# Kernel tuning notes

Hardware: AMD Instinct MI355X
Metric: run time of the kernel (lower is better)

## Reference

```python
import jax, jax.numpy as jnp
import numpy as np

N_NODE = 100000
N_EDGE = 1600000
D_FEAT = 32
DEPTH = 10
BASE_ALPHA = 1.0


def setup_inputs() -> dict:
    key = jax.random.key(0)
    k1, k2, k3, k4 = jax.random.split(key, 4)
    x = jax.random.normal(k1, (N_NODE, D_FEAT), dtype=jnp.float32)
    edge_index = jax.random.randint(k2, (2, N_EDGE), 0, N_NODE, dtype=jnp.int64)
    edge_attr = jax.random.uniform(k3, (N_EDGE,), dtype=jnp.float32)
    pe_alphas = jax.random.normal(k4, (DEPTH,), dtype=jnp.float32)
    return {"x": x, "edge_index": edge_index, "edge_attr": edge_attr, "pe_alphas": pe_alphas}


def reference(x, edge_index, edge_attr, pe_alphas):
    n = x.shape[0]
    row, col = edge_index[0], edge_index[1]
    # GCN normalization: deg from row (source of each edge), clamp isolated nodes
    deg = jax.ops.segment_sum(jnp.ones_like(edge_attr), row, num_segments=n)
    deg = jnp.where(deg < 0.5, deg + 1.0, deg)
    dinv = deg ** -0.5
    val = dinv[row] * edge_attr * dinv[col]  # [E]

    alphas = BASE_ALPHA * jnp.tanh(pe_alphas)  # [DEPTH]

    def spmm(h):  # adj @ h via gather + segment-sum scatter
        return jax.ops.segment_sum(val[:, None] * h[col], row, num_segments=n)

    # PowerConv (monomial basis): x_L = alpha_{L-1} * (adj @ x_{L-1}), x_0 = x
    def step(h, a):
        nh = a * spmm(h)
        return nh, nh

    _, ys = jax.lax.scan(step, x, alphas)  # ys: [DEPTH, n, d]
    out = jnp.concatenate([x[None], ys], axis=0)  # [DEPTH+1, n, d]
    return jnp.moveaxis(out, 0, 1)  # [n, DEPTH+1, d]
```

## Files before the change

### kernel.cpp

```cpp
#include <hip/hip_runtime.h>

#define NN 100000
#define NE 1600000
#define DF 32
#define DEPTH 10
#define LSTRIDE ((DEPTH + 1) * DF)
#define SCAN_BLOCKS 256
#define SCAN_T 256
#define PAD 8
#define PADM (~(PAD - 1))

__global__ void zcnt_k(int* __restrict__ cnt, int n4) {
    int i = blockIdx.x * blockDim.x + threadIdx.x;
    if (i < n4) ((int4*)cnt)[i] = make_int4(0, 0, 0, 0);
}

__global__ void hist_k(const int* __restrict__ row, int* __restrict__ cnt,
                       int* __restrict__ prank, int e) {
    int i = blockIdx.x * blockDim.x + threadIdx.x;
    int stride = gridDim.x * blockDim.x;
    for (; i < e; i += stride) {
        int r = __builtin_nontemporal_load(&row[i]);
        prank[i] = atomicAdd(&cnt[r], 1);
    }
}

__global__ void scan_partial_k(const int* __restrict__ cnt, int* __restrict__ bsum,
                               int n, int chunk) {
    __shared__ int red[SCAN_T];
    int b = blockIdx.x, t = threadIdx.x;
    int beg = b * chunk, end = min(n, beg + chunk);
    int s = 0;
    for (int i = beg + t; i < end; i += SCAN_T) s += (cnt[i] + PAD - 1) & PADM;
    red[t] = s;
    __syncthreads();
    for (int off = SCAN_T / 2; off; off >>= 1) {
        if (t < off) red[t] += red[t + off];
        __syncthreads();
    }
    if (t == 0) bsum[b] = red[0];
}

__global__ void scan_bsum_k(const int* __restrict__ bsum, int* __restrict__ boff) {
    __shared__ int s[SCAN_BLOCKS];
    int t = threadIdx.x;
    s[t] = bsum[t];
    __syncthreads();
    for (int off = 1; off < SCAN_BLOCKS; off <<= 1) {
        int v = (t >= off) ? s[t - off] : 0;
        __syncthreads();
        s[t] += v;
        __syncthreads();
    }
    boff[t] = (t == 0) ? 0 : s[t - 1];
}

__global__ void scan_emit_k(const int* __restrict__ cnt, const int* __restrict__ boff,
                            int* __restrict__ rowptr, float* __restrict__ dinv,
                            int n, int chunk) {
    __shared__ int tile[SCAN_T];
    int b = blockIdx.x, t = threadIdx.x;
    int beg = b * chunk, end = min(n, beg + chunk);
    int run = boff[b];
    for (int base = beg; base < end; base += SCAN_T) {
        int i = base + t;
        int creal = (i < end) ? cnt[i] : 0;
        int c = (creal + PAD - 1) & PADM;
        tile[t] = c;
        __syncthreads();
        for (int off = 1; off < SCAN_T; off <<= 1) {
            int v = (t >= off) ? tile[t - off] : 0;
            __syncthreads();
            tile[t] += v;
            __syncthreads();
        }
        if (i < end) {
            rowptr[i] = run + tile[t] - c;
            float d = (creal == 0) ? 1.0f : (float)creal;
            dinv[i] = rsqrtf(d);
        }
        run += tile[SCAN_T - 1];
        __syncthreads();
    }
    if (b == gridDim.x - 1 && t == 0) rowptr[n] = run;
}

__global__ void pad_k(const int* __restrict__ rowptr, const int* __restrict__ cnt,
                      unsigned long long* __restrict__ cpack, int n) {
    int r = blockIdx.x * blockDim.x + threadIdx.x;
    if (r < n) {
        int p = rowptr[r] + cnt[r];
        int end = rowptr[r + 1];
        for (; p < end; ++p) cpack[p] = 0ull;
    }
}

__global__ void scatter_k(const int* __restrict__ row, const int* __restrict__ col,
                          const float* __restrict__ ea, const float* __restrict__ dinv,
                          const int* __restrict__ rowptr, const int* __restrict__ prank,
                          unsigned long long* __restrict__ cpack, int e) {
    int i = blockIdx.x * blockDim.x + threadIdx.x;
    int stride = gridDim.x * blockDim.x;
    for (; i < e; i += stride) {
        int r = __builtin_nontemporal_load(&row[i]);
        int c = __builtin_nontemporal_load(&col[i]);
        float a = __builtin_nontemporal_load(&ea[i]);
        int pr = __builtin_nontemporal_load(&prank[i]);
        float v = dinv[r] * a * dinv[c];
        int pos = rowptr[r] + pr;
        cpack[pos] = ((unsigned long long)(unsigned)__float_as_int(v) << 32) | (unsigned)c;
    }
}

__global__ void copy_k(const float* __restrict__ x, float* __restrict__ out, int n) {
    int t = blockIdx.x * blockDim.x + threadIdx.x;
    if (t < n * 8) {
        int node = t >> 3, q = t & 7;
        ((float4*)out)[(size_t)node * (LSTRIDE / 4) + q] = ((const float4*)x)[t];
    }
}

__global__ __launch_bounds__(256) void spmm_k(const int* __restrict__ rowptr,
                                              const unsigned long long* __restrict__ cpack,
                                              const float* __restrict__ pe,
                                              float* __restrict__ out, int n, int layer) {
    int gid = blockIdx.x * 8 + (threadIdx.x >> 5);
    int lane = threadIdx.x & 31;
    if (gid >= n) return;
    float alpha = tanhf(pe[layer]);
    const float* __restrict__ hsrc = out + (size_t)layer * DF + lane;
    int beg = rowptr[gid], end = rowptr[gid + 1];
    float acc = 0.f;
    for (int base = beg; base < end; base += 8) {
        unsigned long long p[8];
#pragma unroll
        for (int u = 0; u < 8; ++u) p[u] = __builtin_nontemporal_load(&cpack[base + u]);
        float h[8];
#pragma unroll
        for (int u = 0; u < 8; ++u)
            h[u] = hsrc[(unsigned)(p[u] & 0xFFFFFFFFu) * (unsigned)LSTRIDE];
#pragma unroll
        for (int u = 0; u < 8; ++u)
            acc = fmaf(__uint_as_float((unsigned)(p[u] >> 32)), h[u], acc);
    }
    out[(size_t)gid * LSTRIDE + (layer + 1) * DF + lane] = alpha * acc;
}

extern "C" void kernel_launch(void* const* d_in, const int* in_sizes, int n_in,
                              void* d_out, int out_size, void* d_ws, size_t ws_size,
                              hipStream_t stream) {
    const float* x  = (const float*)d_in[0];
    const int*   ei = (const int*)d_in[1];
    const float* ea = (const float*)d_in[2];
    const float* pe = (const float*)d_in[3];
    float* out = (float*)d_out;

    const int n = in_sizes[0] / DF;
    const int e = in_sizes[2];
    const int* row = ei;
    const int* col = ei + e;

    int*   cnt    = (int*)d_ws;
    int*   rowptr = cnt + n;
    float* dinv   = (float*)(rowptr + n + 1);
    int*   bsum   = (int*)(dinv + n);
    int*   boff   = bsum + SCAN_BLOCKS;
    int*   prank  = boff + SCAN_BLOCKS;
    size_t off = ((size_t)(prank + e) - (size_t)d_ws + 15) & ~(size_t)15;
    unsigned long long* cpack = (unsigned long long*)((char*)d_ws + off);

    const int n4_cnt = (n + 3) / 4;
    const int chunk = (n + SCAN_BLOCKS - 1) / SCAN_BLOCKS;

    zcnt_k<<<(n4_cnt + 255) / 256, 256, 0, stream>>>(cnt, n4_cnt);
    hist_k<<<2048, 256, 0, stream>>>(row, cnt, prank, e);
    scan_partial_k<<<SCAN_BLOCKS, SCAN_T, 0, stream>>>(cnt, bsum, n, chunk);
    scan_bsum_k<<<1, SCAN_BLOCKS, 0, stream>>>(bsum, boff);
    scan_emit_k<<<SCAN_BLOCKS, SCAN_T, 0, stream>>>(cnt, boff, rowptr, dinv, n, chunk);
    pad_k<<<(n + 255) / 256, 256, 0, stream>>>(rowptr, cnt, cpack, n);
    scatter_k<<<2048, 256, 0, stream>>>(row, col, ea, dinv, rowptr, prank, cpack, e);
    copy_k<<<(n * 8 + 255) / 256, 256, 0, stream>>>(x, out, n);

    for (int L = 0; L < DEPTH; ++L) {
        spmm_k<<<(n + 7) / 8, 256, 0, stream>>>(rowptr, cpack, pe, out, n, L);
    }
}
```

Before: 533.1 us.

## Remap SpMM to 64-lane wavefront per row with float4 gathers over 8 edges

```diff
diff --git a/kernel.cpp b/kernel.cpp
--- a/kernel.cpp
+++ b/kernel.cpp
@@ -124,26 +124,35 @@
                                               const unsigned long long* __restrict__ cpack,
                                               const float* __restrict__ pe,
                                               float* __restrict__ out, int n, int layer) {
-    int gid = blockIdx.x * 8 + (threadIdx.x >> 5);
-    int lane = threadIdx.x & 31;
+    int lane = threadIdx.x & 63;
+    int gid = blockIdx.x * 4 + (threadIdx.x >> 6);
     if (gid >= n) return;
+    int eg = lane >> 3, fq = lane & 7;
     float alpha = tanhf(pe[layer]);
-    const float* __restrict__ hsrc = out + (size_t)layer * DF + lane;
+    const float* __restrict__ hsrc = out + (size_t)layer * DF + fq * 4;
     int beg = rowptr[gid], end = rowptr[gid + 1];
-    float acc = 0.f;
+    float4 acc = make_float4(0.f, 0.f, 0.f, 0.f);
     for (int base = beg; base < end; base += 8) {
-        unsigned long long p[8];
+        unsigned long long p = __builtin_nontemporal_load(&cpack[base + eg]);
+        unsigned col = (unsigned)(p & 0xFFFFFFFFu);
+        float val = __uint_as_float((unsigned)(p >> 32));
+        const float4 h4 = *(const float4*)(hsrc + col * (unsigned)LSTRIDE);
+        acc.x = fmaf(val, h4.x, acc.x);
+        acc.y = fmaf(val, h4.y, acc.y);
+        acc.z = fmaf(val, h4.z, acc.z);
+        acc.w = fmaf(val, h4.w, acc.w);
+    }
 #pragma unroll
-        for (int u = 0; u < 8; ++u) p[u] = __builtin_nontemporal_load(&cpack[base + u]);
-        float h[8];
-#pragma unroll
-        for (int u = 0; u < 8; ++u)
-            h[u] = hsrc[(unsigned)(p[u] & 0xFFFFFFFFu) * (unsigned)LSTRIDE];
-#pragma unroll
-        for (int u = 0; u < 8; ++u)
-            acc = fmaf(__uint_as_float((unsigned)(p[u] >> 32)), h[u], acc);
+    for (int s = 8; s < 64; s <<= 1) {
+        acc.x += __shfl_xor(acc.x, s);
+        acc.y += __shfl_xor(acc.y, s);
+        acc.z += __shfl_xor(acc.z, s);
+        acc.w += __shfl_xor(acc.w, s);
     }
-    out[(size_t)gid * LSTRIDE + (layer + 1) * DF + lane] = alpha * acc;
+    if (eg == 0) {
+        float4 r = make_float4(alpha * acc.x, alpha * acc.y, alpha * acc.z, alpha * acc.w);
+        *(float4*)&out[(size_t)gid * LSTRIDE + (layer + 1) * DF + fq * 4] = r;
+    }
 }
 
 extern "C" void kernel_launch(void* const* d_in, const int* in_sizes, int n_in,
@@ -182,6 +191,6 @@
     copy_k<<<(n * 8 + 255) / 256, 256, 0, stream>>>(x, out, n);
 
     for (int L = 0; L < DEPTH; ++L) {
-        spmm_k<<<(n + 7) / 8, 256, 0, stream>>>(rowptr, cpack, pe, out, n, L);
+        spmm_k<<<(n + 3) / 4, 256, 0, stream>>>(rowptr, cpack, pe, out, n, L);
     }
 }
```

Result: slower. 630.8 us (+18.3%).
